# Optimization experiments

Hardware: AMD Instinct MI355X
Metric: run time of the kernel (lower is better)

## Reference

```python
import jax, jax.numpy as jnp
import numpy as np

DIM = 1024
N_HEAD = 16
DIM_HEAD = DIM // N_HEAD
B, L = 4, 2048


def setup_inputs() -> dict:
    key = jax.random.key(0)
    k1, k2, k3, k4, k5 = jax.random.split(key, 5)
    scale = 1.0 / np.sqrt(DIM)
    return {
        "x": jax.random.normal(k1, (B, L, DIM), dtype=jnp.float32),
        "qkv_w": jax.random.normal(k2, (3 * DIM, DIM), dtype=jnp.float32) * scale,
        "qkv_b": jax.random.normal(k3, (3 * DIM,), dtype=jnp.float32) * 0.02,
        "out_w": jax.random.normal(k4, (DIM, DIM), dtype=jnp.float32) * scale,
        "out_b": jax.random.normal(k5, (DIM,), dtype=jnp.float32) * 0.02,
    }


def reference(x, qkv_w, qkv_b, out_w, out_b):
    batch, length, dim = x.shape
    # qkv projection: torch Linear is x @ W.T + b
    qkv = x @ qkv_w.T + qkv_b  # [B, L, 3*dim]
    qkv = qkv.reshape(batch, length, 3, N_HEAD, DIM_HEAD)
    qkv = jnp.transpose(qkv, (2, 0, 3, 1, 4))  # [3, B, H, L, Dh]
    q, k, v = qkv[0], qkv[1], qkv[2]
    attn = jnp.einsum("bhqd,bhkd->bhqk", q, k) / jnp.sqrt(jnp.float32(DIM_HEAD))
    attn = jax.nn.softmax(attn, axis=-1)  # dropout=0 -> identity
    out = jnp.einsum("bhqk,bhkd->bhqd", attn, v)  # [B, H, L, Dh]
    out = jnp.transpose(out, (0, 2, 1, 3)).reshape(batch, length, dim)
    return out @ out_w.T + out_b
```

## Files before the change

### kernel.cpp

```cpp
#include <hip/hip_runtime.h>
#include <math.h>
#include <stdint.h>

typedef __bf16 bf16;
typedef __bf16 bf16x4 __attribute__((ext_vector_type(4)));
typedef __bf16 bf16x8 __attribute__((ext_vector_type(8)));
typedef float f32x4 __attribute__((ext_vector_type(4)));

#define DIMT 1024
#define NH 16
#define DH 64
#define BATCH 4
#define SEQ 2048
#define M_TOT (BATCH*SEQ)

#define SCQ 0.18033688011112042f

__global__ void detect_kernel(const uint16_t* __restrict__ xbits, int* flag) {
    __shared__ int cnt;
    if (threadIdx.x == 0) cnt = 0;
    __syncthreads();
    int local = 0;
    for (int i = threadIdx.x; i < 16384; i += 256) {
        const uint16_t v = xbits[i];
        if ((v & 0x7F80) == 0x7F80) local++;
    }
    atomicAdd(&cnt, local);
    __syncthreads();
    if (threadIdx.x == 0) *flag = (cnt > 0) ? 1 : 0;
}

#define V8_X   1048576L
#define V8_WQ  393216L
#define V8_BQ  384L
#define V8_WO  131072L
#define V8_BO  128L
#define V8_C0  (V8_X)
#define V8_C1  (V8_C0 + V8_WQ)
#define V8_C2  (V8_C1 + V8_BQ)
#define V8_C3  (V8_C2 + V8_WO)
#define V8_TOT (V8_C3 + V8_BO)

__global__ void cvt_all_kernel(const void* __restrict__ s0, const void* __restrict__ s1,
                               const void* __restrict__ s2, const void* __restrict__ s3,
                               const void* __restrict__ s4,
                               bf16* __restrict__ dst, const int* __restrict__ flag) {
    const bool f32 = (*flag != 0);
    const long stride = (long)gridDim.x * blockDim.x;
    for (long v = (long)blockIdx.x * blockDim.x + threadIdx.x; v < V8_TOT; v += stride) {
        const void* src; long off;
        if (v < V8_C0)      { src = s0; off = v; }
        else if (v < V8_C1) { src = s1; off = v - V8_C0; }
        else if (v < V8_C2) { src = s2; off = v - V8_C1; }
        else if (v < V8_C3) { src = s3; off = v - V8_C2; }
        else                { src = s4; off = v - V8_C3; }
        if (f32) {
            const float4 a = ((const float4*)src)[off * 2];
            const float4 b = ((const float4*)src)[off * 2 + 1];
            bf16x8 r;
            r[0] = (bf16)a.x; r[1] = (bf16)a.y; r[2] = (bf16)a.z; r[3] = (bf16)a.w;
            r[4] = (bf16)b.x; r[5] = (bf16)b.y; r[6] = (bf16)b.z; r[7] = (bf16)b.w;
            *(bf16x8*)(dst + v * 8) = r;
        } else {
            *(bf16x8*)(dst + v * 8) = ((const bf16x8*)src)[off];
        }
    }
}

__global__ __launch_bounds__(512, 2) void gemm_qkv_256(
    const bf16* __restrict__ A, const bf16* __restrict__ W,
    const bf16* __restrict__ bias, int K,
    bf16* __restrict__ Qo, bf16* __restrict__ Ko, bf16* __restrict__ Vo)
{
    __shared__ __align__(16) bf16 As[256 * 64];
    __shared__ __align__(16) bf16 Bs[128 * 64];

    const int tid = threadIdx.x;
    const int w = tid >> 6, lane = tid & 63;
    const int lane15 = lane & 15, quad = lane >> 4;
    const int wr = w >> 1, wc = w & 1;

    const int lin = blockIdx.y * gridDim.x + blockIdx.x;
    const int xcd = lin & 7;
    const int j5 = lin >> 3;
    const int m0 = (xcd * 4 + (j5 & 3)) * 256;
    const int n0 = (j5 >> 2) * 128;

    const int trow = tid >> 3, t7 = tid & 7;
    const int csw = t7 ^ (trow & 7);
    const bf16* ag[4]; const bf16* wg[2];
    #pragma unroll
    for (int j = 0; j < 4; j++)
        ag[j] = A + (long)(m0 + j * 64 + trow) * K + csw * 8;
    #pragma unroll
    for (int j = 0; j < 2; j++)
        wg[j] = W + (long)(n0 + j * 64 + trow) * K + csw * 8;
    const int lo = tid * 8;

    const int r7 = lane15 & 7;
    int abase[4], bbase[4];
    #pragma unroll
    for (int i = 0; i < 4; i++) {
        abase[i] = ((wr * 8 + i * 2) + (lane15 >> 3)) * 512 + r7 * 64;
        bbase[i] = ((wc * 8 + i * 2) + (lane15 >> 3)) * 512 + r7 * 64;
    }

    f32x4 acc[4][4] = {};
    for (int k0 = 0; k0 < K; k0 += 64) {
        __syncthreads();
        #pragma unroll
        for (int j = 0; j < 4; j++)
            __builtin_amdgcn_global_load_lds(
                (const __attribute__((address_space(1))) void*)(ag[j] + k0),
                (__attribute__((address_space(3))) void*)(As + j * 4096 + lo), 16, 0, 0);
        #pragma unroll
        for (int j = 0; j < 2; j++)
            __builtin_amdgcn_global_load_lds(
                (const __attribute__((address_space(1))) void*)(wg[j] + k0),
                (__attribute__((address_space(3))) void*)(Bs + j * 4096 + lo), 16, 0, 0);
        __syncthreads();

        #pragma unroll
        for (int ks = 0; ks < 2; ks++) {
            bf16x8 af[4], bfr[4];
            #pragma unroll
            for (int i = 0; i < 4; i++)
                af[i] = *(const bf16x8*)&As[abase[i] + (((ks * 4 + quad) ^ r7) * 8)];
            #pragma unroll
            for (int i = 0; i < 4; i++)
                bfr[i] = *(const bf16x8*)&Bs[bbase[i] + (((ks * 4 + quad) ^ r7) * 8)];
            #pragma unroll
            for (int i = 0; i < 4; i++)
                #pragma unroll
                for (int jj = 0; jj < 4; jj++)
                    acc[i][jj] = __builtin_amdgcn_mfma_f32_16x16x32_bf16(af[i], bfr[jj], acc[i][jj], 0, 0, 0);
        }
    }

    const bool vblock = (n0 >= 2 * DIMT);

    #pragma unroll
    for (int i = 0; i < 4; i++)
    #pragma unroll
    for (int jj = 0; jj < 4; jj++) {
        const int colg = n0 + wc * 64 + jj * 16 + lane15;
        const float bb = (float)bias[colg];
        const int rbase = m0 + wr * 64 + i * 16 + quad * 4;
        if (vblock) {
            const int rem = colg & 1023;
            const int h = rem >> 6, dh = rem & 63;
            const int b = rbase >> 11, l = rbase & 2047;
            const int bh = b * NH + h;
            bf16x4 pv;
            #pragma unroll
            for (int r = 0; r < 4; r++) pv[r] = (bf16)(acc[i][jj][r] + bb);
            *(bf16x4*)&Vo[((long)bh * DH + dh) * SEQ + l] = pv;
        } else {
            #pragma unroll
            for (int r = 0; r < 4; r++) {
                const int rowg = rbase + r;
                float val = acc[i][jj][r] + bb;
                const int which = colg >> 10;
                const int rem = colg & 1023;
                const int h = rem >> 6, dh = rem & 63;
                const int b = rowg >> 11, l = rowg & 2047;
                if (which == 0) val *= SCQ;
                bf16* dst = (which == 0) ? Qo : Ko;
                dst[(((long)(b * NH + h)) * SEQ + l) * DH + dh] = (bf16)val;
            }
        }
    }
}

template<bool QKV>
__global__ __launch_bounds__(256) void gemm_nt_128(
    const bf16* __restrict__ A, const bf16* __restrict__ W,
    const bf16* __restrict__ bias,
    float* __restrict__ CoutF, bf16* __restrict__ CoutH,
    const int* __restrict__ flag,
    int N, int K,
    bf16* __restrict__ Qo, bf16* __restrict__ Ko, bf16* __restrict__ Vo)
{
    __shared__ __align__(16) bf16 As[128 * 64];
    __shared__ __align__(16) bf16 Bs[128 * 64];

    const int tid = threadIdx.x;
    const int w = tid >> 6, lane = tid & 63;
    const int lane15 = lane & 15, quad = lane >> 4;
    const int wr = w >> 1, wc = w & 1;

    const int lin = blockIdx.y * gridDim.x + blockIdx.x;
    const int xcd = lin & 7;
    const int j5 = lin >> 3;
    const int m0 = (xcd * 8 + (j5 & 7)) * 128;
    const int n0 = (j5 >> 3) * 128;

    const int rs = lane >> 3;
    const int c8sw = (lane & 7) ^ rs;
    const bf16* ag[4]; const bf16* wg[4]; int lo[4];
    #pragma unroll
    for (int j = 0; j < 4; j++) {
        const int s = j * 4 + w;
        ag[j] = A + (long)(m0 + s * 8 + rs) * K + c8sw * 8;
        wg[j] = W + (long)(n0 + s * 8 + rs) * K + c8sw * 8;
        lo[j] = s * 512 + lane * 8;
    }

    const int r7 = lane15 & 7;
    int abase[4], bbase[4];
    #pragma unroll
    for (int i = 0; i < 4; i++) {
        abase[i] = ((wr * 8 + i * 2) + (lane15 >> 3)) * 512 + r7 * 64;
        bbase[i] = ((wc * 8 + i * 2) + (lane15 >> 3)) * 512 + r7 * 64;
    }

    f32x4 acc[4][4] = {};
    for (int k0 = 0; k0 < K; k0 += 64) {
        __syncthreads();
        #pragma unroll
        for (int j = 0; j < 4; j++) {
            __builtin_amdgcn_global_load_lds(
                (const __attribute__((address_space(1))) void*)(ag[j] + k0),
                (__attribute__((address_space(3))) void*)(As + lo[j]), 16, 0, 0);
            __builtin_amdgcn_global_load_lds(
                (const __attribute__((address_space(1))) void*)(wg[j] + k0),
                (__attribute__((address_space(3))) void*)(Bs + lo[j]), 16, 0, 0);
        }
        __syncthreads();

        #pragma unroll
        for (int ks = 0; ks < 2; ks++) {
            bf16x8 af[4], bfr[4];
            #pragma unroll
            for (int i = 0; i < 4; i++)
                af[i] = *(const bf16x8*)&As[abase[i] + (((ks * 4 + quad) ^ r7) * 8)];
            #pragma unroll
            for (int i = 0; i < 4; i++)
                bfr[i] = *(const bf16x8*)&Bs[bbase[i] + (((ks * 4 + quad) ^ r7) * 8)];
            #pragma unroll
            for (int i = 0; i < 4; i++)
                #pragma unroll
                for (int jj = 0; jj < 4; jj++)
                    acc[i][jj] = __builtin_amdgcn_mfma_f32_16x16x32_bf16(af[i], bfr[jj], acc[i][jj], 0, 0, 0);
        }
    }

    const bool f32out = QKV ? false : (*flag != 0);
    const bool vblock = QKV && (n0 >= 2 * DIMT);

    #pragma unroll
    for (int i = 0; i < 4; i++)
    #pragma unroll
    for (int jj = 0; jj < 4; jj++) {
        const int colg = n0 + wc * 64 + jj * 16 + lane15;
        const float bb = (float)bias[colg];
        const int rbase = m0 + wr * 64 + i * 16 + quad * 4;
        if (QKV && vblock) {
            const int rem = colg & 1023;
            const int h = rem >> 6, dh = rem & 63;
            const int b = rbase >> 11, l = rbase & 2047;
            const int bh = b * NH + h;
            bf16x4 pv;
            #pragma unroll
            for (int r = 0; r < 4; r++) pv[r] = (bf16)(acc[i][jj][r] + bb);
            *(bf16x4*)&Vo[((long)bh * DH + dh) * SEQ + l] = pv;
        } else {
            #pragma unroll
            for (int r = 0; r < 4; r++) {
                const int rowg = rbase + r;
                float val = acc[i][jj][r] + bb;
                if (QKV) {
                    const int which = colg >> 10;
                    const int rem = colg & 1023;
                    const int h = rem >> 6, dh = rem & 63;
                    const int b = rowg >> 11, l = rowg & 2047;
                    if (which == 0) val *= SCQ;
                    bf16* dst = (which == 0) ? Qo : Ko;
                    dst[(((long)(b * NH + h)) * SEQ + l) * DH + dh] = (bf16)val;
                } else {
                    const long idx = (long)rowg * N + colg;
                    if (f32out) CoutF[idx] = val;
                    else        CoutH[idx] = (bf16)val;
                }
            }
        }
    }
}

__global__ __launch_bounds__(512, 4) void attn_kernel(
    const bf16* __restrict__ Q, const bf16* __restrict__ K,
    const bf16* __restrict__ V, bf16* __restrict__ O)
{
    __shared__ __align__(16) bf16 Ks[2][64 * 64];
    __shared__ __align__(16) bf16 Vts[2][64 * 64];

    const int tid = threadIdx.x;
    const int wave = tid >> 6, lane = tid & 63;
    const int lane15 = lane & 15, quad = lane >> 4;
    const int bh = blockIdx.x;
    const int b = bh >> 4, h = bh & 15;
    const int q0 = blockIdx.y * 256;

    const bf16* Qb = Q + (long)bh * SEQ * DH;
    const bf16* Kb = K + (long)bh * SEQ * DH;
    const bf16* Vb = V + (long)bh * DH * SEQ;

    bf16x8 qf[2][2];
    #pragma unroll
    for (int ms = 0; ms < 2; ms++) {
        const long qr = q0 + wave * 32 + ms * 16 + lane15;
        qf[ms][0] = *(const bf16x8*)(Qb + qr * DH + quad * 8);
        qf[ms][1] = *(const bf16x8*)(Qb + qr * DH + 32 + quad * 8);
    }

    bf16x8 ones;
    #pragma unroll
    for (int e = 0; e < 8; e++) ones[e] = (bf16)1.0f;

    f32x4 o_acc[2][4] = {};
    f32x4 o_l[2] = {};

    const int l8 = lane >> 3, l7b = lane & 7;
    const int c8sw = l7b ^ l8;
    const int srow = wave * 8 + l8;
    const int gkey = (((srow >> 4) & 1) << 5) | (((srow >> 2) & 3) << 3)
                   | ((srow >> 5) << 2) | (srow & 3);
    const int ldso = wave * 512 + lane * 8;
    const bf16* kgp = Kb + (long)gkey * DH + c8sw * 8;
    const bf16* vgp = Vb + (long)srow * SEQ + c8sw * 8;

    const int r7 = lane15 & 7;

    auto STAGE = [&](int kt, int bi) {
        __builtin_amdgcn_global_load_lds(
            (const __attribute__((address_space(1))) void*)(kgp + (long)kt * (64 * DH)),
            (__attribute__((address_space(3))) void*)(&Ks[bi][ldso]), 16, 0, 0);
        __builtin_amdgcn_global_load_lds(
            (const __attribute__((address_space(1))) void*)(vgp + kt * 64),
            (__attribute__((address_space(3))) void*)(&Vts[bi][ldso]), 16, 0, 0);
    };

    auto TILE = [&](const bf16* KsB, const bf16* VtB) {
        __builtin_amdgcn_s_setprio(1);
        f32x4 sT[2][4];
        #pragma unroll
        for (int kn = 0; kn < 4; kn++) {
            const int krow = kn * 16 + lane15;
            bf16x8 k0 = *(const bf16x8*)&KsB[krow * 64 + ((quad ^ r7) * 8)];
            bf16x8 k1 = *(const bf16x8*)&KsB[krow * 64 + (((4 + quad) ^ r7) * 8)];
            #pragma unroll
            for (int ms = 0; ms < 2; ms++) {
                f32x4 a = {};
                a = __builtin_amdgcn_mfma_f32_16x16x32_bf16(k0, qf[ms][0], a, 0, 0, 0);
                a = __builtin_amdgcn_mfma_f32_16x16x32_bf16(k1, qf[ms][1], a, 0, 0, 0);
                sT[ms][kn] = a;
            }
        }

        bf16x8 pf[2][2];
        #pragma unroll
        for (int ms = 0; ms < 2; ms++) {
            #pragma unroll
            for (int hh = 0; hh < 2; hh++) {
                bf16x8 p;
                #pragma unroll
                for (int j = 0; j < 8; j++)
                    p[j] = (bf16)__builtin_amdgcn_exp2f(sT[ms][2 * (j >> 2) + hh][j & 3]);
                pf[ms][hh] = p;
            }
            o_l[ms] = __builtin_amdgcn_mfma_f32_16x16x32_bf16(pf[ms][0], ones, o_l[ms], 0, 0, 0);
            o_l[ms] = __builtin_amdgcn_mfma_f32_16x16x32_bf16(pf[ms][1], ones, o_l[ms], 0, 0, 0);
        }

        #pragma unroll
        for (int dn = 0; dn < 4; dn++) {
            const int vrow = dn * 16 + lane15;
            bf16x8 vf0 = *(const bf16x8*)&VtB[vrow * 64 + ((quad ^ r7) * 8)];
            bf16x8 vf1 = *(const bf16x8*)&VtB[vrow * 64 + (((4 + quad) ^ r7) * 8)];
            #pragma unroll
            for (int ms = 0; ms < 2; ms++) {
                o_acc[ms][dn] = __builtin_amdgcn_mfma_f32_16x16x32_bf16(pf[ms][0], vf0, o_acc[ms][dn], 0, 0, 0);
                o_acc[ms][dn] = __builtin_amdgcn_mfma_f32_16x16x32_bf16(pf[ms][1], vf1, o_acc[ms][dn], 0, 0, 0);
            }
        }
        __builtin_amdgcn_s_setprio(0);
    };

    STAGE(0, 0);
    __syncthreads();
    for (int kt = 0; kt < SEQ / 64; kt += 2) {
        STAGE(kt + 1, 1);
        TILE(&Ks[0][0], &Vts[0][0]);
        __syncthreads();
        if (kt + 2 < SEQ / 64) STAGE(kt + 2, 0);
        TILE(&Ks[1][0], &Vts[1][0]);
        __syncthreads();
    }

    #pragma unroll
    for (int ms = 0; ms < 2; ms++) {
        float rcl[4];
        #pragma unroll
        for (int r = 0; r < 4; r++) rcl[r] = 1.0f / o_l[ms][r];
        #pragma unroll
        for (int dn = 0; dn < 4; dn++)
            #pragma unroll
            for (int r = 0; r < 4; r++) {
                const int rowl = q0 + wave * 32 + ms * 16 + quad * 4 + r;
                const int col = h * DH + dn * 16 + lane15;
                O[((long)b * SEQ + rowl) * DIMT + col] = (bf16)(o_acc[ms][dn][r] * rcl[r]);
            }
    }
}

extern "C" void kernel_launch(void* const* d_in, const int* in_sizes, int n_in,
                              void* d_out, int out_size, void* d_ws, size_t ws_size,
                              hipStream_t stream) {
    const void* x     = d_in[0];
    const void* qkv_w = d_in[1];
    const void* qkv_b = d_in[2];
    const void* out_w = d_in[3];
    const void* out_b = d_in[4];

    const long n_x  = (long)M_TOT * DIMT;
    const long n_wq = 3L * DIMT * DIMT;
    const long n_bq = 3L * DIMT;
    const long n_wo = (long)DIMT * DIMT;
    const long n_bo = DIMT;

    int* flag = (int*)d_ws;
    bf16* xb = (bf16*)((char*)d_ws + 64);
    bf16* wq = xb + n_x;
    bf16* bq = wq + n_wq;
    bf16* wo = bq + n_bq;
    bf16* bo = wo + n_wo;
    bf16* qb = bo + n_bo;
    bf16* kb = qb + n_x;
    bf16* vb = kb + n_x;
    bf16* ob = vb + n_x;

    detect_kernel<<<1, 256, 0, stream>>>((const uint16_t*)x, flag);
    cvt_all_kernel<<<2048, 256, 0, stream>>>(x, qkv_w, qkv_b, out_w, out_b, xb, flag);

    dim3 g1(3 * DIMT / 128, M_TOT / 256);
    gemm_qkv_256<<<g1, 512, 0, stream>>>(xb, wq, bq, DIMT, qb, kb, vb);

    dim3 g2(BATCH * NH, SEQ / 256);
    attn_kernel<<<g2, 512, 0, stream>>>(qb, kb, vb, ob);

    dim3 g3(DIMT / 128, M_TOT / 128);
    gemm_nt_128<false><<<g3, 256, 0, stream>>>(ob, wo, bo,
                                               (float*)d_out, (bf16*)d_out, flag,
                                               DIMT, DIMT, qb, kb, vb);
}
```

Measured before the change: 277.3 us.

## Double-buffer QKV GEMM LDS tiles with BK=32 to overlap loads and MFMA

The QKV projection GEMM now splits its LDS staging into two buffers of half the K-depth (32 instead of 64). The next tile's global-to-LDS load is issued before computing on the current tile, so memory traffic overlaps with MFMA work, and there is now one barrier per K step. Total LDS use stays the same, but the swizzle pattern and address math change, and each barrier covers half as much compute.

```diff
diff --git a/kernel.cpp b/kernel.cpp
--- a/kernel.cpp
+++ b/kernel.cpp
@@ -72,8 +72,8 @@
     const bf16* __restrict__ bias, int K,
     bf16* __restrict__ Qo, bf16* __restrict__ Ko, bf16* __restrict__ Vo)
 {
-    __shared__ __align__(16) bf16 As[256 * 64];
-    __shared__ __align__(16) bf16 Bs[128 * 64];
+    __shared__ __align__(16) bf16 As[2][256 * 32];
+    __shared__ __align__(16) bf16 Bs[2][128 * 32];
 
     const int tid = threadIdx.x;
     const int w = tid >> 6, lane = tid & 63;
@@ -86,55 +86,61 @@
     const int m0 = (xcd * 4 + (j5 & 3)) * 256;
     const int n0 = (j5 >> 2) * 128;
 
-    const int trow = tid >> 3, t7 = tid & 7;
-    const int csw = t7 ^ (trow & 7);
-    const bf16* ag[4]; const bf16* wg[2];
-    #pragma unroll
-    for (int j = 0; j < 4; j++)
-        ag[j] = A + (long)(m0 + j * 64 + trow) * K + csw * 8;
+    const int trow = tid >> 2;
+    const int csw = (tid & 3) ^ ((tid >> 3) & 3);
+    const bf16* ag[2]; const bf16* wg;
     #pragma unroll
     for (int j = 0; j < 2; j++)
-        wg[j] = W + (long)(n0 + j * 64 + trow) * K + csw * 8;
+        ag[j] = A + (long)(m0 + j * 128 + trow) * K + csw * 8;
+    wg = W + (long)(n0 + trow) * K + csw * 8;
     const int lo = tid * 8;
 
-    const int r7 = lane15 & 7;
+    const int r3w = (lane15 >> 1) & 3;
     int abase[4], bbase[4];
     #pragma unroll
     for (int i = 0; i < 4; i++) {
-        abase[i] = ((wr * 8 + i * 2) + (lane15 >> 3)) * 512 + r7 * 64;
-        bbase[i] = ((wc * 8 + i * 2) + (lane15 >> 3)) * 512 + r7 * 64;
+        abase[i] = (wr * 64 + i * 16 + lane15) * 32;
+        bbase[i] = (wc * 64 + i * 16 + lane15) * 32;
     }
 
     f32x4 acc[4][4] = {};
-    for (int k0 = 0; k0 < K; k0 += 64) {
-        __syncthreads();
-        #pragma unroll
-        for (int j = 0; j < 4; j++)
+
+    auto STAGE = [&](int k0, int bi) {
+        #pragma unroll
+        for (int j = 0; j < 2; j++)
             __builtin_amdgcn_global_load_lds(
                 (const __attribute__((address_space(1))) void*)(ag[j] + k0),
-                (__attribute__((address_space(3))) void*)(As + j * 4096 + lo), 16, 0, 0);
-        #pragma unroll
-        for (int j = 0; j < 2; j++)
-            __builtin_amdgcn_global_load_lds(
-                (const __attribute__((address_space(1))) void*)(wg[j] + k0),
-                (__attribute__((address_space(3))) void*)(Bs + j * 4096 + lo), 16, 0, 0);
-        __syncthreads();
-
-        #pragma unroll
-        for (int ks = 0; ks < 2; ks++) {
-            bf16x8 af[4], bfr[4];
-            #pragma unroll
-            for (int i = 0; i < 4; i++)
-                af[i] = *(const bf16x8*)&As[abase[i] + (((ks * 4 + quad) ^ r7) * 8)];
-            #pragma unroll
-            for (int i = 0; i < 4; i++)
-                bfr[i] = *(const bf16x8*)&Bs[bbase[i] + (((ks * 4 + quad) ^ r7) * 8)];
-            #pragma unroll
-            for (int i = 0; i < 4; i++)
-                #pragma unroll
-                for (int jj = 0; jj < 4; jj++)
-                    acc[i][jj] = __builtin_amdgcn_mfma_f32_16x16x32_bf16(af[i], bfr[jj], acc[i][jj], 0, 0, 0);
-        }
+                (__attribute__((address_space(3))) void*)(&As[bi][j * 4096 + lo]), 16, 0, 0);
+        __builtin_amdgcn_global_load_lds(
+            (const __attribute__((address_space(1))) void*)(wg + k0),
+            (__attribute__((address_space(3))) void*)(&Bs[bi][lo]), 16, 0, 0);
+    };
+
+    auto COMPUTE = [&](const bf16* AsB, const bf16* BsB) {
+        bf16x8 af[4], bfr[4];
+        #pragma unroll
+        for (int i = 0; i < 4; i++)
+            af[i] = *(const bf16x8*)&AsB[abase[i] + ((quad ^ r3w) * 8)];
+        #pragma unroll
+        for (int i = 0; i < 4; i++)
+            bfr[i] = *(const bf16x8*)&BsB[bbase[i] + ((quad ^ r3w) * 8)];
+        #pragma unroll
+        for (int i = 0; i < 4; i++)
+            #pragma unroll
+            for (int jj = 0; jj < 4; jj++)
+                acc[i][jj] = __builtin_amdgcn_mfma_f32_16x16x32_bf16(af[i], bfr[jj], acc[i][jj], 0, 0, 0);
+    };
+
+    const int nk = K >> 5;
+    STAGE(0, 0);
+    __syncthreads();
+    for (int t = 0; t < nk; t += 2) {
+        STAGE((t + 1) << 5, 1);
+        COMPUTE(&As[0][0], &Bs[0][0]);
+        __syncthreads();
+        if (t + 2 < nk) STAGE((t + 2) << 5, 0);
+        COMPUTE(&As[1][0], &Bs[1][0]);
+        __syncthreads();
     }
 
     const bool vblock = (n0 >= 2 * DIMT);
```

After: 274.6 us. About the same (-1.0%).
